# Optimization experiments

Measured on AMD Instinct MI355X. Metric: run time of the kernel, lower is better.

The kernel has to match this reference:

```python
import jax, jax.numpy as jnp
import numpy as np

D_MODEL = 1024
HEAD_SIZE = 64
BLOCK_SIZE = 2048
B, T = 4, 2048


def setup_inputs() -> dict:
    key = jax.random.key(0)
    ks = jax.random.split(key, 7)
    s = 1.0 / np.sqrt(D_MODEL)
    x = jax.random.normal(ks[0], (B, T, D_MODEL), dtype=jnp.float32)
    Wq = jax.random.uniform(ks[1], (D_MODEL, HEAD_SIZE), jnp.float32, -s, s)
    bq = jax.random.uniform(ks[2], (HEAD_SIZE,), jnp.float32, -s, s)
    Wk = jax.random.uniform(ks[3], (D_MODEL, HEAD_SIZE), jnp.float32, -s, s)
    bk = jax.random.uniform(ks[4], (HEAD_SIZE,), jnp.float32, -s, s)
    Wv = jax.random.uniform(ks[5], (D_MODEL, HEAD_SIZE), jnp.float32, -s, s)
    return {"x": x, "Wq": Wq, "bq": bq, "Wk": Wk, "bk": bk, "Wv": Wv, "mask": 1}


def reference(x, Wq, bq, Wk, bk, Wv, mask):
    # x: [B, T, C]; single attention head, dropout is identity (eval/p=0)
    Tlen = x.shape[1]
    q = x @ Wq + bq              # [B, T, hs]
    k = x @ Wk + bk              # [B, T, hs]
    v = x @ Wv                   # [B, T, hs] (no bias)
    hs = k.shape[-1]
    # Faithful to source: weights = QK^T / hs**(-0.5)  ==  QK^T * sqrt(hs)
    w = jnp.einsum('btd,bsd->bts', q, k) * jnp.sqrt(jnp.asarray(hs, x.dtype))
    if mask:
        causal = jnp.tril(jnp.ones((Tlen, Tlen), dtype=bool))
        w = jnp.where(causal, w, jnp.asarray(-jnp.inf, w.dtype))
    w = jax.nn.softmax(w, axis=-1)
    out = jnp.einsum('bts,bsd->btd', w, v)  # [B, T, hs]
    return out
```

## Files before the change

kernel.cpp:

```cpp
#include <hip/hip_runtime.h>
#include <hip/hip_bf16.h>

#define D_MODEL 1024
#define HS 64
#define T_LEN 2048
#define JCH 256
#define NCH 8

typedef __attribute__((ext_vector_type(8))) short bf16x8;
typedef __attribute__((ext_vector_type(4))) float f32x4;

__device__ inline void split8(const float* v, int4& hi, int4& lo) {
    union { unsigned short u[8]; int4 v4; } uh, ul;
    #pragma unroll
    for (int i = 0; i < 8; ++i) {
        const unsigned int b = __float_as_uint(v[i]);
        const unsigned short h = (unsigned short)(b >> 16);
        const float r = v[i] - __uint_as_float((unsigned int)h << 16);
        uh.u[i] = h;
        ul.u[i] = (unsigned short)(__float_as_uint(r) >> 16);
    }
    hi = uh.v4; lo = ul.v4;
}

__device__ inline unsigned short f2bf_rne(float f) {
    const unsigned int b = __float_as_uint(f);
    return (unsigned short)((b + 0x7FFFu + ((b >> 16) & 1u)) >> 16);
}
__device__ inline float bf2f(unsigned short h) {
    return __uint_as_float((unsigned int)h << 16);
}

__device__ inline void async_copy16(const short* g, short* l) {
    __builtin_amdgcn_global_load_lds(
        (const __attribute__((address_space(1))) void*)g,
        (__attribute__((address_space(3))) void*)l, 16, 0, 0);
}

__global__ __launch_bounds__(256) void prep_kernel(
    const float* __restrict__ x,
    const float* __restrict__ Wq, const float* __restrict__ Wk,
    const float* __restrict__ Wv,
    short* __restrict__ xh, short* __restrict__ xl,
    short* __restrict__ wh, short* __restrict__ wl, int BT)
{
    __shared__ float tile[64][69];
    const int tid = threadIdx.x;
    const int bx  = blockIdx.x;
    const int nxb = BT >> 4;

    if (bx < nxb) {
        const int mtg = bx;
        #pragma unroll
        for (int i = 0; i < 8; ++i) {
            const int s    = tid + 256 * i;
            const int kc   = s >> 6;
            const int lane = s & 63;
            const float* src = x + (size_t)(mtg * 16 + (lane & 15)) * D_MODEL
                                 + kc * 32 + (lane >> 4) * 8;
            float v[8];
            *(float4*)&v[0] = *(const float4*)src;
            *(float4*)&v[4] = *(const float4*)(src + 4);
            int4 hi, lo;
            split8(v, hi, lo);
            const size_t off = ((size_t)(mtg * 32 + kc) * 64 + lane) * 8;
            *(int4*)(xh + off) = hi;
            *(int4*)(xl + off) = lo;
        }
    } else {
        const int wb = bx - nxb;
        const int kb = wb & 15;
        const int m  = wb >> 4;
        const float* W = (m == 0) ? Wq : (m == 1) ? Wk : Wv;
        #pragma unroll
        for (int it = 0; it < 4; ++it) {
            const int idx = tid + 256 * it;
            const int kr = idx >> 4, c4 = idx & 15;
            *(float4*)&tile[kr][4 * c4] =
                *(const float4*)(W + (size_t)(kb * 64 + kr) * HS + 4 * c4);
        }
        __syncthreads();
        #pragma unroll
        for (int i = 0; i < 2; ++i) {
            const int s    = tid + 256 * i;
            const int ntl  = s >> 7;
            const int kcl  = (s >> 6) & 1;
            const int lane = s & 63;
            const int n    = ntl * 16 + (lane & 15);
            const int krel = kcl * 32 + (lane >> 4) * 8;
            float v[8];
            #pragma unroll
            for (int e = 0; e < 8; ++e) v[e] = tile[krel + e][n];
            int4 hi, lo;
            split8(v, hi, lo);
            const size_t off =
                ((size_t)((m * 4 + ntl) * 32 + kb * 2 + kcl) * 64 + lane) * 8;
            *(int4*)(wh + off) = hi;
            *(int4*)(wl + off) = lo;
        }
    }
}

__global__ __launch_bounds__(256) void qkv_kernel(
    const short* __restrict__ xh, const short* __restrict__ xl,
    const short* __restrict__ wh, const short* __restrict__ wl,
    const float* __restrict__ bq, const float* __restrict__ bk,
    short* __restrict__ qfh, short* __restrict__ qfl,
    short* __restrict__ kfh, short* __restrict__ kfl, short* __restrict__ vf,
    int BT)
{
    __shared__ __align__(16) short A_lds[8 * 512];
    __shared__ __align__(16) short B_lds[16 * 512];

    const int tid  = threadIdx.x;
    const int r0   = blockIdx.x * 32;
    const int nb   = blockIdx.y;
    const int wave = tid >> 6;
    const int lane = tid & 63;
    const int mt_w = wave >> 1;
    const int nt0  = (wave & 1) * 2;

    f32x4 acc0 = (f32x4)(0.f);
    f32x4 acc1 = (f32x4)(0.f);

    const size_t mtg0 = (size_t)(r0 >> 4);
    const size_t ntg0 = (size_t)(nb * 4);

    for (int k0 = 0; k0 < D_MODEL; k0 += 64) {
        const int kc0 = k0 >> 5;
        __syncthreads();
        #pragma unroll
        for (int ii = 0; ii < 6; ++ii) {
            const int g = wave * 6 + ii;
            if (g < 8) {
                const int mt = g >> 2, kcl = (g >> 1) & 1, p = g & 1;
                const short* base = p ? xl : xh;
                const short* gsrc = base + ((mtg0 + mt) * 32 + kc0 + kcl) * 512;
                async_copy16(gsrc + lane * 8, &A_lds[g * 512]);
            } else {
                const int gb = g - 8;
                const int nt = gb >> 2, kcl = (gb >> 1) & 1, p = gb & 1;
                const short* base = p ? wl : wh;
                const short* gsrc = base + ((ntg0 + nt) * 32 + kc0 + kcl) * 512;
                async_copy16(gsrc + lane * 8, &B_lds[gb * 512]);
            }
        }
        __syncthreads();
        #pragma unroll
        for (int kcl = 0; kcl < 2; ++kcl) {
            const bf16x8 afh = *(const bf16x8*)&A_lds[(mt_w * 4 + kcl * 2 + 0) * 512 + lane * 8];
            const bf16x8 afl = *(const bf16x8*)&A_lds[(mt_w * 4 + kcl * 2 + 1) * 512 + lane * 8];
            {
                const bf16x8 bfh = *(const bf16x8*)&B_lds[(nt0 * 4 + kcl * 2 + 0) * 512 + lane * 8];
                const bf16x8 bfl = *(const bf16x8*)&B_lds[(nt0 * 4 + kcl * 2 + 1) * 512 + lane * 8];
                acc0 = __builtin_amdgcn_mfma_f32_16x16x32_bf16(afh, bfh, acc0, 0, 0, 0);
                acc0 = __builtin_amdgcn_mfma_f32_16x16x32_bf16(afh, bfl, acc0, 0, 0, 0);
                acc0 = __builtin_amdgcn_mfma_f32_16x16x32_bf16(afl, bfh, acc0, 0, 0, 0);
            }
            {
                const bf16x8 bfh = *(const bf16x8*)&B_lds[((nt0 + 1) * 4 + kcl * 2 + 0) * 512 + lane * 8];
                const bf16x8 bfl = *(const bf16x8*)&B_lds[((nt0 + 1) * 4 + kcl * 2 + 1) * 512 + lane * 8];
                acc1 = __builtin_amdgcn_mfma_f32_16x16x32_bf16(afh, bfh, acc1, 0, 0, 0);
                acc1 = __builtin_amdgcn_mfma_f32_16x16x32_bf16(afh, bfl, acc1, 0, 0, 0);
                acc1 = __builtin_amdgcn_mfma_f32_16x16x32_bf16(afl, bfh, acc1, 0, 0, 0);
            }
        }
    }

    const int rowb = r0 + mt_w * 16 + (lane >> 4) * 4;
    #pragma unroll
    for (int j = 0; j < 2; ++j) {
        const f32x4 a = (j == 0) ? acc0 : acc1;
        const int c = nb * 64 + (nt0 + j) * 16 + (lane & 15);
        if (c < 128) {
            const int cc    = (c < 64) ? c : (c - 64);
            const float bias = (c < 64) ? bq[cc] : bk[cc];
            short* dsth = (c < 64) ? qfh : kfh;
            short* dstl = (c < 64) ? qfl : kfl;
            const int tile16 = rowb >> 4;
            const int kc2   = cc >> 5;
            const int quadd = (cc & 31) >> 3;
            const int e     = cc & 7;
            #pragma unroll
            for (int r = 0; r < 4; ++r) {
                const float val = a[r] + bias;
                const unsigned int b = __float_as_uint(val);
                const unsigned short h = (unsigned short)(b >> 16);
                const float res = val - __uint_as_float((unsigned int)h << 16);
                const unsigned short l16 = (unsigned short)(__float_as_uint(res) >> 16);
                const int laned = ((rowb + r) & 15) | (quadd << 4);
                const size_t off = ((size_t)((tile16 * 2 + kc2) * 64 + laned)) * 8 + e;
                dsth[off] = (short)h;
                dstl[off] = (short)l16;
            }
        } else {
            const int cv    = c - 128;
            const int vb    = rowb >> 6;
            const int jc2   = (rowb & 63) >> 5;
            const int quadd = (rowb & 31) >> 3;
            const int gg    = jc2 * 4 + (cv >> 4);
            const int laned = (cv & 15) | (quadd << 4);
            const size_t base = ((size_t)((vb * 8 + gg) * 64 + laned)) * 8 + (rowb & 7);
            short4 pk;
            pk.x = (short)f2bf_rne(a[0]);
            pk.y = (short)f2bf_rne(a[1]);
            pk.z = (short)f2bf_rne(a[2]);
            pk.w = (short)f2bf_rne(a[3]);
            *(short4*)(vf + base) = pk;
        }
    }
}

__global__ __launch_bounds__(256) void attn_kernel(
    const short* __restrict__ qfh, const short* __restrict__ qfl,
    const short* __restrict__ kfh, const short* __restrict__ kfl,
    const short* __restrict__ vf, const int* __restrict__ maskp,
    float* __restrict__ part_O, float* __restrict__ part_ml, int BT)
{
    __shared__ __align__(16) short Kh[4096], Kl[4096];
    __shared__ __align__(16) short Vt[4096];
    __shared__ __align__(16) short Pl[4][16 * 72];

    const int tile  = blockIdx.x;
    const int chunk = blockIdx.y;
    const int r0 = tile * 64;
    const int tb = r0 / T_LEN;
    const int t0 = r0 - tb * T_LEN;
    const int mask = (*maskp != 0);
    const int n_max = mask ? (t0 + 64) : T_LEN;
    const int j0 = chunk * JCH;
    if (j0 >= n_max) return;
    const int hi_j = min(j0 + JCH, n_max);
    const int njt = (hi_j - j0 + 63) >> 6;

    const int tid  = threadIdx.x;
    const int w    = tid >> 6;
    const int lane = tid & 63;
    const int quad = lane >> 4;
    const int l15  = lane & 15;
    const int rw0  = t0 + 16 * w;
    const int rowa = r0 + 16 * w + quad * 4;

    bf16x8 qh[2], ql[2];
    {
        const size_t qt = (size_t)(r0 >> 4) + w;
        #pragma unroll
        for (int kc = 0; kc < 2; ++kc) {
            qh[kc] = *(const bf16x8*)&qfh[((qt * 2 + kc) * 64 + lane) * 8];
            ql[kc] = *(const bf16x8*)&qfl[((qt * 2 + kc) * 64 + lane) * 8];
        }
    }

    f32x4 oacc[4];
    #pragma unroll
    for (int nt = 0; nt < 4; ++nt) oacc[nt] = (f32x4)(0.f);
    float m_r[4] = {-INFINITY, -INFINITY, -INFINITY, -INFINITY};
    float l_r[4] = {0.f, 0.f, 0.f, 0.f};

    for (int jt = 0; jt < njt; ++jt) {
        const int jbase = j0 + jt * 64;
        __syncthreads();
        {
            const size_t kt0 = (size_t)(tb * 128) + (jbase >> 4);
            const size_t vb  = (size_t)(tb * 32) + (jbase >> 6);
            #pragma unroll
            for (int ii = 0; ii < 6; ++ii) {
                const int g = w * 6 + ii;
                if (g < 8) {
                    const short* src = kfh + ((kt0 + (g >> 1)) * 2 + (g & 1)) * 512;
                    async_copy16(src + lane * 8, &Kh[g * 512]);
                } else if (g < 16) {
                    const int gg = g - 8;
                    const short* src = kfl + ((kt0 + (gg >> 1)) * 2 + (gg & 1)) * 512;
                    async_copy16(src + lane * 8, &Kl[gg * 512]);
                } else {
                    const int gg = g - 16;
                    const short* src = vf + (vb * 8 + gg) * 512;
                    async_copy16(src + lane * 8, &Vt[gg * 512]);
                }
            }
        }
        __syncthreads();

        const bool active = (!mask) || (jbase <= rw0 + 15);
        if (active) {
            f32x4 sacc[4];
            #pragma unroll
            for (int jsub = 0; jsub < 4; ++jsub) {
                f32x4 s = (f32x4)(0.f);
                #pragma unroll
                for (int kc = 0; kc < 2; ++kc) {
                    const bf16x8 kh = *(const bf16x8*)&Kh[((jsub * 2 + kc) * 64 + lane) * 8];
                    const bf16x8 kl = *(const bf16x8*)&Kl[((jsub * 2 + kc) * 64 + lane) * 8];
                    s = __builtin_amdgcn_mfma_f32_16x16x32_bf16(qh[kc], kh, s, 0, 0, 0);
                    s = __builtin_amdgcn_mfma_f32_16x16x32_bf16(qh[kc], kl, s, 0, 0, 0);
                    s = __builtin_amdgcn_mfma_f32_16x16x32_bf16(ql[kc], kh, s, 0, 0, 0);
                }
                sacc[jsub] = s;
            }
            float sval[4][4], rmax[4];
            #pragma unroll
            for (int r = 0; r < 4; ++r) rmax[r] = -INFINITY;
            #pragma unroll
            for (int jsub = 0; jsub < 4; ++jsub) {
                const int jg = jbase + jsub * 16 + l15;
                #pragma unroll
                for (int r = 0; r < 4; ++r) {
                    const int tg = rw0 + quad * 4 + r;
                    const float vv = (mask && (jg > tg)) ? -INFINITY : 8.0f * sacc[jsub][r];
                    sval[jsub][r] = vv;
                    rmax[r] = fmaxf(rmax[r], vv);
                }
            }
            #pragma unroll
            for (int d = 1; d < 16; d <<= 1)
                #pragma unroll
                for (int r = 0; r < 4; ++r)
                    rmax[r] = fmaxf(rmax[r], __shfl_xor(rmax[r], d));
            float alpha[4], msafe[4];
            #pragma unroll
            for (int r = 0; r < 4; ++r) {
                const float mn = fmaxf(m_r[r], rmax[r]);
                msafe[r] = (mn == -INFINITY) ? 0.f : mn;
                alpha[r] = __expf(m_r[r] - msafe[r]);
                m_r[r] = mn;
            }
            short* Pw = &Pl[w][0];
            float rsum[4] = {0.f, 0.f, 0.f, 0.f};
            #pragma unroll
            for (int jsub = 0; jsub < 4; ++jsub) {
                #pragma unroll
                for (int r = 0; r < 4; ++r) {
                    const float e = __expf(sval[jsub][r] - msafe[r]);
                    const unsigned short eb = f2bf_rne(e);
                    Pw[(quad * 4 + r) * 72 + jsub * 16 + l15] = (short)eb;
                    rsum[r] += bf2f(eb);
                }
            }
            #pragma unroll
            for (int d = 1; d < 16; d <<= 1)
                #pragma unroll
                for (int r = 0; r < 4; ++r)
                    rsum[r] += __shfl_xor(rsum[r], d);
            #pragma unroll
            for (int r = 0; r < 4; ++r)
                l_r[r] = l_r[r] * alpha[r] + rsum[r];
            #pragma unroll
            for (int nt = 0; nt < 4; ++nt)
                #pragma unroll
                for (int r = 0; r < 4; ++r)
                    oacc[nt][r] *= alpha[r];
            bf16x8 pf[2];
            #pragma unroll
            for (int jc = 0; jc < 2; ++jc)
                pf[jc] = *(const bf16x8*)&Pw[l15 * 72 + jc * 32 + quad * 8];
            #pragma unroll
            for (int nt = 0; nt < 4; ++nt) {
                #pragma unroll
                for (int jc = 0; jc < 2; ++jc) {
                    const bf16x8 vfr = *(const bf16x8*)&Vt[((jc * 4 + nt) * 64 + lane) * 8];
                    oacc[nt] = __builtin_amdgcn_mfma_f32_16x16x32_bf16(pf[jc], vfr, oacc[nt], 0, 0, 0);
                }
            }
        }
    }

    #pragma unroll
    for (int nt = 0; nt < 4; ++nt)
        #pragma unroll
        for (int r = 0; r < 4; ++r)
            part_O[((size_t)(rowa + r) * NCH + chunk) * HS + nt * 16 + l15] = oacc[nt][r];
    if (l15 == 0) {
        #pragma unroll
        for (int r = 0; r < 4; ++r) {
            float2 ml;
            ml.x = m_r[r];
            ml.y = l_r[r];
            *(float2*)(part_ml + ((size_t)(rowa + r) * NCH + chunk) * 2) = ml;
        }
    }
}

__global__ __launch_bounds__(256) void combine_kernel(
    const float* __restrict__ part_O, const float* __restrict__ part_ml,
    const int* __restrict__ maskp, float* __restrict__ out)
{
    const int f = blockIdx.x * 256 + threadIdx.x;
    const int row = f >> 4;
    const int d4 = (f & 15) * 4;
    const int t = row & (T_LEN - 1);
    const int mask = (*maskp != 0);
    const int n = mask ? (t + 1) : T_LEN;
    const int nc = (n + JCH - 1) / JCH;

    const float2* mlp = (const float2*)(part_ml + (size_t)row * NCH * 2);
    float M = -INFINITY;
    for (int c = 0; c < nc; ++c) M = fmaxf(M, mlp[c].x);
    float L = 0.f;
    float Ox = 0.f, Oy = 0.f, Oz = 0.f, Ow = 0.f;
    for (int c = 0; c < nc; ++c) {
        const float2 ml = mlp[c];
        const float w = __expf(ml.x - M);
        L += ml.y * w;
        const float4 p = *(const float4*)(part_O + ((size_t)row * NCH + c) * HS + d4);
        Ox = fmaf(p.x, w, Ox);
        Oy = fmaf(p.y, w, Oy);
        Oz = fmaf(p.z, w, Oz);
        Ow = fmaf(p.w, w, Ow);
    }
    float4 res;
    res.x = Ox / L;
    res.y = Oy / L;
    res.z = Oz / L;
    res.w = Ow / L;
    *(float4*)(out + (size_t)row * HS + d4) = res;
}

extern "C" void kernel_launch(void* const* d_in, const int* in_sizes, int n_in,
                              void* d_out, int out_size, void* d_ws, size_t ws_size,
                              hipStream_t stream) {
    const float* x  = (const float*)d_in[0];
    const float* Wq = (const float*)d_in[1];
    const float* bq = (const float*)d_in[2];
    const float* Wk = (const float*)d_in[3];
    const float* bk = (const float*)d_in[4];
    const float* Wv = (const float*)d_in[5];
    const int* maskp = (const int*)d_in[6];

    const int BT = in_sizes[0] / D_MODEL;

    float* pO  = (float*)d_ws;
    float* pml = pO + (size_t)BT * NCH * HS;
    short* xh  = (short*)(pml + (size_t)BT * NCH * 2);
    short* xl  = xh + (size_t)BT * D_MODEL;
    short* wh  = xl + (size_t)BT * D_MODEL;
    short* wl  = wh + (size_t)192 * D_MODEL;
    short* qfh = wl + (size_t)192 * D_MODEL;
    short* qfl = qfh + (size_t)BT * HS;
    short* kfh = qfl + (size_t)BT * HS;
    short* kfl = kfh + (size_t)BT * HS;
    short* vf  = kfl + (size_t)BT * HS;

    prep_kernel<<<BT / 16 + 48, 256, 0, stream>>>(x, Wq, Wk, Wv, xh, xl, wh, wl, BT);
    dim3 qgrid(BT / 32, 3);
    qkv_kernel<<<qgrid, 256, 0, stream>>>(xh, xl, wh, wl, bq, bk,
                                          qfh, qfl, kfh, kfl, vf, BT);
    dim3 agrid(BT / 64, NCH);
    attn_kernel<<<agrid, 256, 0, stream>>>(qfh, qfl, kfh, kfl, vf, maskp,
                                           pO, pml, BT);
    combine_kernel<<<(BT * 16) / 256, 256, 0, stream>>>(pO, pml, maskp, (float*)d_out);
}
```

Baseline: 137.8 us.

## Fuse x bf16 split into QKV GEMM with double-buffered pipelined loads

```diff
diff --git a/kernel.cpp b/kernel.cpp
--- a/kernel.cpp
+++ b/kernel.cpp
@@ -38,175 +38,181 @@
 }
 
 __global__ __launch_bounds__(256) void prep_kernel(
-    const float* __restrict__ x,
     const float* __restrict__ Wq, const float* __restrict__ Wk,
     const float* __restrict__ Wv,
-    short* __restrict__ xh, short* __restrict__ xl,
-    short* __restrict__ wh, short* __restrict__ wl, int BT)
+    short* __restrict__ wh, short* __restrict__ wl)
 {
     __shared__ float tile[64][69];
     const int tid = threadIdx.x;
-    const int bx  = blockIdx.x;
-    const int nxb = BT >> 4;
-
-    if (bx < nxb) {
-        const int mtg = bx;
-        #pragma unroll
-        for (int i = 0; i < 8; ++i) {
-            const int s    = tid + 256 * i;
-            const int kc   = s >> 6;
-            const int lane = s & 63;
-            const float* src = x + (size_t)(mtg * 16 + (lane & 15)) * D_MODEL
-                                 + kc * 32 + (lane >> 4) * 8;
-            float v[8];
-            *(float4*)&v[0] = *(const float4*)src;
-            *(float4*)&v[4] = *(const float4*)(src + 4);
-            int4 hi, lo;
-            split8(v, hi, lo);
-            const size_t off = ((size_t)(mtg * 32 + kc) * 64 + lane) * 8;
-            *(int4*)(xh + off) = hi;
-            *(int4*)(xl + off) = lo;
-        }
-    } else {
-        const int wb = bx - nxb;
-        const int kb = wb & 15;
-        const int m  = wb >> 4;
-        const float* W = (m == 0) ? Wq : (m == 1) ? Wk : Wv;
-        #pragma unroll
-        for (int it = 0; it < 4; ++it) {
-            const int idx = tid + 256 * it;
-            const int kr = idx >> 4, c4 = idx & 15;
-            *(float4*)&tile[kr][4 * c4] =
-                *(const float4*)(W + (size_t)(kb * 64 + kr) * HS + 4 * c4);
-        }
-        __syncthreads();
-        #pragma unroll
-        for (int i = 0; i < 2; ++i) {
-            const int s    = tid + 256 * i;
-            const int ntl  = s >> 7;
-            const int kcl  = (s >> 6) & 1;
-            const int lane = s & 63;
-            const int n    = ntl * 16 + (lane & 15);
-            const int krel = kcl * 32 + (lane >> 4) * 8;
-            float v[8];
-            #pragma unroll
-            for (int e = 0; e < 8; ++e) v[e] = tile[krel + e][n];
-            int4 hi, lo;
-            split8(v, hi, lo);
-            const size_t off =
-                ((size_t)((m * 4 + ntl) * 32 + kb * 2 + kcl) * 64 + lane) * 8;
-            *(int4*)(wh + off) = hi;
-            *(int4*)(wl + off) = lo;
-        }
+    const int wb  = blockIdx.x;
+    const int kb  = wb & 15;
+    const int m   = wb >> 4;
+    const float* W = (m == 0) ? Wq : (m == 1) ? Wk : Wv;
+    #pragma unroll
+    for (int it = 0; it < 4; ++it) {
+        const int idx = tid + 256 * it;
+        const int kr = idx >> 4, c4 = idx & 15;
+        *(float4*)&tile[kr][4 * c4] =
+            *(const float4*)(W + (size_t)(kb * 64 + kr) * HS + 4 * c4);
+    }
+    __syncthreads();
+    #pragma unroll
+    for (int i = 0; i < 2; ++i) {
+        const int s    = tid + 256 * i;
+        const int ntl  = s >> 7;
+        const int kcl  = (s >> 6) & 1;
+        const int lane = s & 63;
+        const int n    = ntl * 16 + (lane & 15);
+        const int krel = kcl * 32 + (lane >> 4) * 8;
+        float v[8];
+        #pragma unroll
+        for (int e = 0; e < 8; ++e) v[e] = tile[krel + e][n];
+        int4 hi, lo;
+        split8(v, hi, lo);
+        const size_t off =
+            ((size_t)((m * 4 + ntl) * 32 + kb * 2 + kcl) * 64 + lane) * 8;
+        *(int4*)(wh + off) = hi;
+        *(int4*)(wl + off) = lo;
+    }
+}
+
+__device__ inline void stage_B(const short* __restrict__ wh,
+                               const short* __restrict__ wl,
+                               short* Bdst, int ch, int wave, int lane) {
+    #pragma unroll
+    for (int ii = 0; ii < 12; ++ii) {
+        const int g   = wave * 12 + ii;
+        const int nt  = g >> 2;
+        const int kcl = (g >> 1) & 1;
+        const int p   = g & 1;
+        const short* src = (p ? wl : wh)
+                         + ((size_t)(nt * 32 + ch * 2 + kcl)) * 512;
+        async_copy16(src + lane * 8, Bdst + g * 512);
     }
 }
 
 __global__ __launch_bounds__(256) void qkv_kernel(
-    const short* __restrict__ xh, const short* __restrict__ xl,
+    const float* __restrict__ x,
     const short* __restrict__ wh, const short* __restrict__ wl,
     const float* __restrict__ bq, const float* __restrict__ bk,
     short* __restrict__ qfh, short* __restrict__ qfl,
-    short* __restrict__ kfh, short* __restrict__ kfl, short* __restrict__ vf,
-    int BT)
+    short* __restrict__ kfh, short* __restrict__ kfl, short* __restrict__ vf)
 {
-    __shared__ __align__(16) short A_lds[8 * 512];
-    __shared__ __align__(16) short B_lds[16 * 512];
-
-    const int tid  = threadIdx.x;
-    const int r0   = blockIdx.x * 32;
-    const int nb   = blockIdx.y;
-    const int wave = tid >> 6;
-    const int lane = tid & 63;
-    const int mt_w = wave >> 1;
-    const int nt0  = (wave & 1) * 2;
-
-    f32x4 acc0 = (f32x4)(0.f);
-    f32x4 acc1 = (f32x4)(0.f);
-
-    const size_t mtg0 = (size_t)(r0 >> 4);
-    const size_t ntg0 = (size_t)(nb * 4);
-
-    for (int k0 = 0; k0 < D_MODEL; k0 += 64) {
-        const int kc0 = k0 >> 5;
+    __shared__ __align__(16) short A_lds[2][8 * 512];
+    __shared__ __align__(16) short B_lds[2][48 * 512];
+
+    const int tid   = threadIdx.x;
+    const int r0    = blockIdx.x * 32;
+    const int wave  = tid >> 6;
+    const int lane  = tid & 63;
+    const int mt_l  = tid >> 7;
+    const int kcl_l = (tid >> 6) & 1;
+    const int nt0   = wave * 3;
+
+    const float* xrow = x + (size_t)(r0 + mt_l * 16 + (lane & 15)) * D_MODEL
+                          + kcl_l * 32 + (lane >> 4) * 8;
+
+    f32x4 acc[2][3];
+    #pragma unroll
+    for (int mt = 0; mt < 2; ++mt)
+        #pragma unroll
+        for (int j = 0; j < 3; ++j) acc[mt][j] = (f32x4)(0.f);
+
+    {
+        stage_B(wh, wl, &B_lds[0][0], 0, wave, lane);
+        float v[8];
+        *(float4*)&v[0] = *(const float4*)(xrow);
+        *(float4*)&v[4] = *(const float4*)(xrow + 4);
+        int4 hi, lo;
+        split8(v, hi, lo);
+        *(int4*)&A_lds[0][(mt_l * 4 + kcl_l * 2 + 0) * 512 + lane * 8] = hi;
+        *(int4*)&A_lds[0][(mt_l * 4 + kcl_l * 2 + 1) * 512 + lane * 8] = lo;
+    }
+    __syncthreads();
+
+    int cur = 0;
+    for (int t = 0; t < 16; ++t) {
+        float v[8];
+        const bool pf = (t < 15);
+        if (pf) {
+            *(float4*)&v[0] = *(const float4*)(xrow + (t + 1) * 64);
+            *(float4*)&v[4] = *(const float4*)(xrow + (t + 1) * 64 + 4);
+            stage_B(wh, wl, &B_lds[cur ^ 1][0], t + 1, wave, lane);
+        }
+        #pragma unroll
+        for (int kcl = 0; kcl < 2; ++kcl) {
+            const bf16x8 a0h = *(const bf16x8*)&A_lds[cur][(0 + kcl * 2 + 0) * 512 + lane * 8];
+            const bf16x8 a0l = *(const bf16x8*)&A_lds[cur][(0 + kcl * 2 + 1) * 512 + lane * 8];
+            const bf16x8 a1h = *(const bf16x8*)&A_lds[cur][(4 + kcl * 2 + 0) * 512 + lane * 8];
+            const bf16x8 a1l = *(const bf16x8*)&A_lds[cur][(4 + kcl * 2 + 1) * 512 + lane * 8];
+            #pragma unroll
+            for (int j = 0; j < 3; ++j) {
+                const int gb = (nt0 + j) * 4 + kcl * 2;
+                const bf16x8 bh = *(const bf16x8*)&B_lds[cur][(gb + 0) * 512 + lane * 8];
+                const bf16x8 bl = *(const bf16x8*)&B_lds[cur][(gb + 1) * 512 + lane * 8];
+                acc[0][j] = __builtin_amdgcn_mfma_f32_16x16x32_bf16(a0h, bh, acc[0][j], 0, 0, 0);
+                acc[0][j] = __builtin_amdgcn_mfma_f32_16x16x32_bf16(a0h, bl, acc[0][j], 0, 0, 0);
+                acc[0][j] = __builtin_amdgcn_mfma_f32_16x16x32_bf16(a0l, bh, acc[0][j], 0, 0, 0);
+                acc[1][j] = __builtin_amdgcn_mfma_f32_16x16x32_bf16(a1h, bh, acc[1][j], 0, 0, 0);
+                acc[1][j] = __builtin_amdgcn_mfma_f32_16x16x32_bf16(a1h, bl, acc[1][j], 0, 0, 0);
+                acc[1][j] = __builtin_amdgcn_mfma_f32_16x16x32_bf16(a1l, bh, acc[1][j], 0, 0, 0);
+            }
+        }
+        if (pf) {
+            int4 hi, lo;
+            split8(v, hi, lo);
+            *(int4*)&A_lds[cur ^ 1][(mt_l * 4 + kcl_l * 2 + 0) * 512 + lane * 8] = hi;
+            *(int4*)&A_lds[cur ^ 1][(mt_l * 4 + kcl_l * 2 + 1) * 512 + lane * 8] = lo;
+        }
         __syncthreads();
-        #pragma unroll
-        for (int ii = 0; ii < 6; ++ii) {
-            const int g = wave * 6 + ii;
-            if (g < 8) {
-                const int mt = g >> 2, kcl = (g >> 1) & 1, p = g & 1;
-                const short* base = p ? xl : xh;
-                const short* gsrc = base + ((mtg0 + mt) * 32 + kc0 + kcl) * 512;
-                async_copy16(gsrc + lane * 8, &A_lds[g * 512]);
+        cur ^= 1;
+    }
+
+    const int quad = lane >> 4;
+    const int l15  = lane & 15;
+    #pragma unroll
+    for (int mt = 0; mt < 2; ++mt) {
+        const int rowb = r0 + mt * 16 + quad * 4;
+        #pragma unroll
+        for (int j = 0; j < 3; ++j) {
+            const f32x4 a = acc[mt][j];
+            const int c = (nt0 + j) * 16 + l15;
+            if (c < 128) {
+                const int cc    = (c < 64) ? c : (c - 64);
+                const float bias = (c < 64) ? bq[cc] : bk[cc];
+                short* dsth = (c < 64) ? qfh : kfh;
+                short* dstl = (c < 64) ? qfl : kfl;
+                const int tile16 = rowb >> 4;
+                const int kc2   = cc >> 5;
+                const int quadd = (cc & 31) >> 3;
+                const int e     = cc & 7;
+                #pragma unroll
+                for (int r = 0; r < 4; ++r) {
+                    const float val = a[r] + bias;
+                    const unsigned int b = __float_as_uint(val);
+                    const unsigned short h = (unsigned short)(b >> 16);
+                    const float res = val - __uint_as_float((unsigned int)h << 16);
+                    const unsigned short l16 = (unsigned short)(__float_as_uint(res) >> 16);
+                    const int laned = ((rowb + r) & 15) | (quadd << 4);
+                    const size_t off = ((size_t)((tile16 * 2 + kc2) * 64 + laned)) * 8 + e;
+                    dsth[off] = (short)h;
+                    dstl[off] = (short)l16;
+                }
             } else {
-                const int gb = g - 8;
-                const int nt = gb >> 2, kcl = (gb >> 1) & 1, p = gb & 1;
-                const short* base = p ? wl : wh;
-                const short* gsrc = base + ((ntg0 + nt) * 32 + kc0 + kcl) * 512;
-                async_copy16(gsrc + lane * 8, &B_lds[gb * 512]);
-            }
-        }
-        __syncthreads();
-        #pragma unroll
-        for (int kcl = 0; kcl < 2; ++kcl) {
-            const bf16x8 afh = *(const bf16x8*)&A_lds[(mt_w * 4 + kcl * 2 + 0) * 512 + lane * 8];
-            const bf16x8 afl = *(const bf16x8*)&A_lds[(mt_w * 4 + kcl * 2 + 1) * 512 + lane * 8];
-            {
-                const bf16x8 bfh = *(const bf16x8*)&B_lds[(nt0 * 4 + kcl * 2 + 0) * 512 + lane * 8];
-                const bf16x8 bfl = *(const bf16x8*)&B_lds[(nt0 * 4 + kcl * 2 + 1) * 512 + lane * 8];
-                acc0 = __builtin_amdgcn_mfma_f32_16x16x32_bf16(afh, bfh, acc0, 0, 0, 0);
-                acc0 = __builtin_amdgcn_mfma_f32_16x16x32_bf16(afh, bfl, acc0, 0, 0, 0);
-                acc0 = __builtin_amdgcn_mfma_f32_16x16x32_bf16(afl, bfh, acc0, 0, 0, 0);
-            }
-            {
-                const bf16x8 bfh = *(const bf16x8*)&B_lds[((nt0 + 1) * 4 + kcl * 2 + 0) * 512 + lane * 8];
-                const bf16x8 bfl = *(const bf16x8*)&B_lds[((nt0 + 1) * 4 + kcl * 2 + 1) * 512 + lane * 8];
-                acc1 = __builtin_amdgcn_mfma_f32_16x16x32_bf16(afh, bfh, acc1, 0, 0, 0);
-                acc1 = __builtin_amdgcn_mfma_f32_16x16x32_bf16(afh, bfl, acc1, 0, 0, 0);
-                acc1 = __builtin_amdgcn_mfma_f32_16x16x32_bf16(afl, bfh, acc1, 0, 0, 0);
-            }
-        }
-    }
-
-    const int rowb = r0 + mt_w * 16 + (lane >> 4) * 4;
-    #pragma unroll
-    for (int j = 0; j < 2; ++j) {
-        const f32x4 a = (j == 0) ? acc0 : acc1;
-        const int c = nb * 64 + (nt0 + j) * 16 + (lane & 15);
-        if (c < 128) {
-            const int cc    = (c < 64) ? c : (c - 64);
-            const float bias = (c < 64) ? bq[cc] : bk[cc];
-            short* dsth = (c < 64) ? qfh : kfh;
-            short* dstl = (c < 64) ? qfl : kfl;
-            const int tile16 = rowb >> 4;
-            const int kc2   = cc >> 5;
-            const int quadd = (cc & 31) >> 3;
-            const int e     = cc & 7;
-            #pragma unroll
-            for (int r = 0; r < 4; ++r) {
-                const float val = a[r] + bias;
-                const unsigned int b = __float_as_uint(val);
-                const unsigned short h = (unsigned short)(b >> 16);
-                const float res = val - __uint_as_float((unsigned int)h << 16);
-                const unsigned short l16 = (unsigned short)(__float_as_uint(res) >> 16);
-                const int laned = ((rowb + r) & 15) | (quadd << 4);
-                const size_t off = ((size_t)((tile16 * 2 + kc2) * 64 + laned)) * 8 + e;
-                dsth[off] = (short)h;
-                dstl[off] = (short)l16;
-            }
-        } else {
-            const int cv    = c - 128;
-            const int vb    = rowb >> 6;
-            const int jc2   = (rowb & 63) >> 5;
-            const int quadd = (rowb & 31) >> 3;
-            const int gg    = jc2 * 4 + (cv >> 4);
-            const int laned = (cv & 15) | (quadd << 4);
-            const size_t base = ((size_t)((vb * 8 + gg) * 64 + laned)) * 8 + (rowb & 7);
-            short4 pk;
-            pk.x = (short)f2bf_rne(a[0]);
-            pk.y = (short)f2bf_rne(a[1]);
-            pk.z = (short)f2bf_rne(a[2]);
-            pk.w = (short)f2bf_rne(a[3]);
-            *(short4*)(vf + base) = pk;
+                const int cv    = c - 128;
+                const int vb    = rowb >> 6;
+                const int jc2   = (rowb & 63) >> 5;
+                const int quadd = (rowb & 31) >> 3;
+                const int gg    = jc2 * 4 + (cv >> 4);
+                const int laned = (cv & 15) | (quadd << 4);
+                const size_t base = ((size_t)((vb * 8 + gg) * 64 + laned)) * 8 + (rowb & 7);
+                short4 pk;
+                pk.x = (short)f2bf_rne(a[0]);
+                pk.y = (short)f2bf_rne(a[1]);
+                pk.z = (short)f2bf_rne(a[2]);
+                pk.w = (short)f2bf_rne(a[3]);
+                *(short4*)(vf + base) = pk;
+            }
         }
     }
 }
@@ -431,9 +437,7 @@
 
     float* pO  = (float*)d_ws;
     float* pml = pO + (size_t)BT * NCH * HS;
-    short* xh  = (short*)(pml + (size_t)BT * NCH * 2);
-    short* xl  = xh + (size_t)BT * D_MODEL;
-    short* wh  = xl + (size_t)BT * D_MODEL;
+    short* wh  = (short*)(pml + (size_t)BT * NCH * 2);
     short* wl  = wh + (size_t)192 * D_MODEL;
     short* qfh = wl + (size_t)192 * D_MODEL;
     short* qfl = qfh + (size_t)BT * HS;
@@ -441,10 +445,9 @@
     short* kfl = kfh + (size_t)BT * HS;
     short* vf  = kfl + (size_t)BT * HS;
 
-    prep_kernel<<<BT / 16 + 48, 256, 0, stream>>>(x, Wq, Wk, Wv, xh, xl, wh, wl, BT);
-    dim3 qgrid(BT / 32, 3);
-    qkv_kernel<<<qgrid, 256, 0, stream>>>(xh, xl, wh, wl, bq, bk,
-                                          qfh, qfl, kfh, kfl, vf, BT);
+    prep_kernel<<<48, 256, 0, stream>>>(Wq, Wk, Wv, wh, wl);
+    qkv_kernel<<<BT / 32, 256, 0, stream>>>(x, wh, wl, bq, bk,
+                                            qfh, qfl, kfh, kfl, vf);
     dim3 agrid(BT / 64, NCH);
     attn_kernel<<<agrid, 256, 0, stream>>>(qfh, qfl, kfh, kfl, vf, maskp,
                                            pO, pml, BT);
```

Result: no change. 138.8 us (+0.7%).
